# Performance work log

Measured on AMD Instinct MI355X. Metric: run time of the kernel, lower is better.

Reference implementation:

```python
import jax, jax.numpy as jnp
import numpy as np
import math

B, N, D, H = 4, 2048, 1024, 16
HD = D // H  # head dim = 64


def setup_inputs() -> dict:
    key = jax.random.key(0)
    ks = jax.random.split(key, 5)
    x = jax.random.normal(ks[0], (B, N, D), dtype=jnp.float32)
    # per-head kqv Linear: weight (3*HD, D), bias (3*HD), stacked over heads
    Wkqv = jax.random.normal(ks[1], (H, 3 * HD, D), dtype=jnp.float32) / math.sqrt(D)
    bkqv = jax.random.normal(ks[2], (H, 3 * HD), dtype=jnp.float32) * 0.02
    # output projection Linear(D, D)
    Wproj = jax.random.normal(ks[3], (D, D), dtype=jnp.float32) / math.sqrt(D)
    bproj = jax.random.normal(ks[4], (D,), dtype=jnp.float32) * 0.02
    return {"x": x, "Wkqv": Wkqv, "bkqv": bkqv, "Wproj": Wproj, "bproj": bproj}


def reference(x, Wkqv, bkqv, Wproj, bproj):
    # per-head linear: y = x @ W.T + b  -> [B, H, N, 3*HD]
    kqv = jnp.einsum('bnd,hed->bhne', x, Wkqv) + bkqv[None, :, None, :]
    k, q, v = jnp.split(kqv, 3, axis=-1)  # each [B, H, N, HD]
    # scores = q @ k^T / sqrt(HD)   (attention_scores(k, q) -> q @ k.T)
    scores = jnp.einsum('bhqd,bhkd->bhqk', q, k) / math.sqrt(HD)
    causal = jnp.tril(jnp.ones((N, N), dtype=bool))
    scores = jnp.where(causal[None, None], scores, -jnp.inf)
    att = jax.nn.softmax(scores, axis=-1)
    out = jnp.einsum('bhqk,bhkd->bhqd', att, v)  # [B, H, N, HD]
    # concat heads: [B, N, H*HD]
    sa = out.transpose(0, 2, 1, 3).reshape(B, N, D)
    # dropout is identity in eval mode; final projection
    return sa @ Wproj.T + bproj
```

## Files before the change

kernel.cpp:

```cpp
#include <hip/hip_runtime.h>
#include <hip/hip_bf16.h>


#define NSEQ 2048
#define NHEAD 16
#define DMODEL 1024
#define SCALE2 0.18033688011112042f

typedef __attribute__((ext_vector_type(8))) short v8s;
typedef __attribute__((ext_vector_type(4))) float v4f;

__device__ __forceinline__ float bf2f(unsigned short u) {
    union { unsigned int i; float f; } v;
    v.i = ((unsigned int)u) << 16;
    return v.f;
}
__device__ __forceinline__ unsigned short f2bf(float f) {
    unsigned int x = __float_as_uint(f);
    return (unsigned short)((x + 0x7fffu + ((x >> 16) & 1u)) >> 16);
}
__device__ __forceinline__ unsigned short f2bf_rh(float f) {
    return (unsigned short)((__float_as_uint(f) + 0x8000u) >> 16);
}
__device__ __forceinline__ float fast_exp2(float x) {
#if __has_builtin(__builtin_amdgcn_exp2f)
    return __builtin_amdgcn_exp2f(x);
#else
    return __expf(x * 0.69314718056f);
#endif
}
__device__ __forceinline__ void gld_lds16(const unsigned short* g, unsigned short* l) {
    __builtin_amdgcn_global_load_lds(
        (const __attribute__((address_space(1))) void*)g,
        (__attribute__((address_space(3))) void*)l, 16, 0, 0);
}

__global__ __launch_bounds__(256) void cvt_bf16(
    const float* __restrict__ x, const float* __restrict__ wk, const float* __restrict__ wp,
    unsigned short* __restrict__ xb, unsigned short* __restrict__ wkb,
    unsigned short* __restrict__ wpb)
{
    const int i = blockIdx.x * 256 + threadIdx.x;
    const float* s; unsigned short* d; int o;
    if (i < 2097152)      { s = x;  d = xb;  o = i; }
    else if (i < 2883584) {
        s = wk; d = wkb;
        const int oi  = i - 2097152;
        const int row = oi >> 8, cq = oi & 255;
        const int h   = row / 192;
        const int rem = row - h * 192;
        const int cls = rem >> 6, e = rem & 63;
        float4 f = ((const float4*)s)[oi];
        ushort4 u;
        u.x = f2bf(f.x); u.y = f2bf(f.y); u.z = f2bf(f.z); u.w = f2bf(f.w);
        ((ushort4*)d)[(((cls << 10) + (h << 6) + e) << 8) + cq] = u;
        return;
    }
    else                  { s = wp; d = wpb; o = i - 2883584; }
    float4 f = ((const float4*)s)[o];
    ushort4 u;
    u.x = f2bf(f.x); u.y = f2bf(f.y); u.z = f2bf(f.z); u.w = f2bf(f.w);
    ((ushort4*)d)[o] = u;
}

template <int EPI>
__global__ __launch_bounds__(256, 3) void gemm_lds(
    const unsigned short* __restrict__ A, const unsigned short* __restrict__ B,
    const float* __restrict__ bias,
    float* __restrict__ Cf,
    unsigned short* __restrict__ Kb, unsigned short* __restrict__ Qb,
    unsigned short* __restrict__ VTb,
    int M, int Nc, int K)
{
    __shared__ __align__(16) unsigned short Al[512 * 8];
    __shared__ __align__(16) unsigned short Bl[512 * 8];

    const int t = threadIdx.x, wave = t >> 6, lane = t & 63;
    const int wm = wave >> 1, wn = wave & 1;
    const int m0 = blockIdx.y * 128, n0 = blockIdx.x * 128;
    const int quad = lane >> 4, c = lane & 15;

    const int g0 = wave * 2, g1 = wave * 2 + 1;
    const int r15 = lane & 15, kg = (lane >> 4) & 3;
    const unsigned short* sA0 = A + (size_t)(m0 + g0 * 16 + r15) * K + kg * 8;
    const unsigned short* sA1 = A + (size_t)(m0 + g1 * 16 + r15) * K + kg * 8;
    const unsigned short* sB0 = B + (size_t)(n0 + g0 * 16 + r15) * K + kg * 8;
    const unsigned short* sB1 = B + (size_t)(n0 + g1 * 16 + r15) * K + kg * 8;
    unsigned short* dA0 = &Al[g0 * 512];
    unsigned short* dA1 = &Al[g1 * 512];
    unsigned short* dB0 = &Bl[g0 * 512];
    unsigned short* dB1 = &Bl[g1 * 512];

    v4f acc[4][4];
#pragma unroll
    for (int i = 0; i < 4; ++i)
#pragma unroll
        for (int j = 0; j < 4; ++j) acc[i][j] = (v4f){0.f, 0.f, 0.f, 0.f};

    const int fbase = (quad * 16 + c) * 8;

    for (int k0 = 0; k0 < K; k0 += 32) {
        __syncthreads();
        gld_lds16(sA0 + k0, dA0);
        gld_lds16(sA1 + k0, dA1);
        gld_lds16(sB0 + k0, dB0);
        gld_lds16(sB1 + k0, dB1);
        __syncthreads();

        v8s af[4], bf[4];
#pragma unroll
        for (int ms = 0; ms < 4; ++ms)
            af[ms] = *(const v8s*)&Al[(wm * 4 + ms) * 512 + fbase];
#pragma unroll
        for (int ns = 0; ns < 4; ++ns)
            bf[ns] = *(const v8s*)&Bl[(wn * 4 + ns) * 512 + fbase];
#pragma unroll
        for (int ms = 0; ms < 4; ++ms)
#pragma unroll
            for (int ns = 0; ns < 4; ++ns)
                acc[ms][ns] = __builtin_amdgcn_mfma_f32_16x16x32_bf16(
                    af[ms], bf[ns], acc[ms][ns], 0, 0, 0);
    }

#pragma unroll
    for (int ms = 0; ms < 4; ++ms) {
        const int row0 = m0 + wm * 64 + ms * 16 + quad * 4;
#pragma unroll
        for (int ns = 0; ns < 4; ++ns) {
            const int colbase = n0 + wn * 64 + ns * 16;
            float bn, scl = 1.f;
            if (EPI == 2) {
                bn = bias[colbase + c];
            } else {
                const int cls = colbase >> 10;
                const int wi  = colbase & 1023;
                const int h   = wi >> 6, e0 = wi & 63;
                bn = bias[h * 192 + cls * 64 + e0 + c];
                if (cls == 1) scl = SCALE2;
            }
            float v0 = (acc[ms][ns][0] + bn) * scl;
            float v1 = (acc[ms][ns][1] + bn) * scl;
            float v2 = (acc[ms][ns][2] + bn) * scl;
            float v3 = (acc[ms][ns][3] + bn) * scl;
            if (EPI == 2) {
                float* pc = Cf + (size_t)row0 * Nc + colbase + c;
                pc[0] = v0; pc[(size_t)Nc] = v1;
                pc[(size_t)2 * Nc] = v2; pc[(size_t)3 * Nc] = v3;
            } else {
                const int cls = colbase >> 10;
                const int wi  = colbase & 1023;
                const int h   = wi >> 6, e = (wi & 63) + c;
                const int bb  = row0 >> 11, tok0 = row0 & 2047;
                const int bhh = bb * 16 + h;
                if (cls == 2) {
                    ushort4 pk;
                    pk.x = f2bf(v0); pk.y = f2bf(v1); pk.z = f2bf(v2); pk.w = f2bf(v3);
                    *(ushort4*)(VTb + ((size_t)bhh * 64 + e) * 2048 + tok0) = pk;
                } else {
                    unsigned short* dst = (cls == 0) ? Kb : Qb;
                    const size_t base = ((size_t)bhh * 2048 + tok0) * 64 + e;
                    dst[base]       = f2bf(v0);
                    dst[base + 64]  = f2bf(v1);
                    dst[base + 128] = f2bf(v2);
                    dst[base + 192] = f2bf(v3);
                }
            }
        }
    }
}

template <bool A_BF16, int EPI>
__global__ __launch_bounds__(256) void gemm_mfma(
    const void* __restrict__ Av, const float* __restrict__ B,
    const float* __restrict__ bias,
    float* __restrict__ Cf,
    unsigned short* __restrict__ Kb, unsigned short* __restrict__ Qb,
    unsigned short* __restrict__ VTb,
    int M, int Nc, int K)
{
    __shared__ __align__(16) unsigned short Al[512 * 8];
    __shared__ __align__(16) unsigned short Bl[512 * 8];

    const int t = threadIdx.x;
    const int wave = t >> 6, lane = t & 63;
    const int wm = wave >> 1, wn = wave & 1;
    const int m0 = blockIdx.y * 128, n0 = blockIdx.x * 128;
    const int quad = lane >> 4, c = lane & 15;

    const int srow = t >> 1, skh = t & 1;
    const int sslot = (srow >> 4) * 64 + (skh * 2) * 16 + (srow & 15);

    v4f acc[4][4];
#pragma unroll
    for (int i = 0; i < 4; ++i)
#pragma unroll
        for (int j = 0; j < 4; ++j) acc[i][j] = (v4f){0.f, 0.f, 0.f, 0.f};

    const unsigned short* pa_u = (const unsigned short*)Av + (size_t)(m0 + srow) * K + skh * 16;
    const float*          pa_f = (const float*)Av          + (size_t)(m0 + srow) * K + skh * 16;
    const float*          pb   = B                          + (size_t)(n0 + srow) * K + skh * 16;

    const int fbase = (quad * 16 + c) * 8;

    for (int k0 = 0; k0 < K; k0 += 32) {
        unsigned short a16[16], b16[16];
        if (A_BF16) {
            uint4 r0 = *(const uint4*)(pa_u + k0);
            uint4 r1 = *(const uint4*)(pa_u + k0 + 8);
            *(uint4*)&a16[0] = r0; *(uint4*)&a16[8] = r1;
        } else {
            float4 f0 = *(const float4*)(pa_f + k0);
            float4 f1 = *(const float4*)(pa_f + k0 + 4);
            float4 f2 = *(const float4*)(pa_f + k0 + 8);
            float4 f3 = *(const float4*)(pa_f + k0 + 12);
            a16[0] = f2bf_rh(f0.x); a16[1] = f2bf_rh(f0.y); a16[2] = f2bf_rh(f0.z); a16[3] = f2bf_rh(f0.w);
            a16[4] = f2bf_rh(f1.x); a16[5] = f2bf_rh(f1.y); a16[6] = f2bf_rh(f1.z); a16[7] = f2bf_rh(f1.w);
            a16[8] = f2bf_rh(f2.x); a16[9] = f2bf_rh(f2.y); a16[10] = f2bf_rh(f2.z); a16[11] = f2bf_rh(f2.w);
            a16[12] = f2bf_rh(f3.x); a16[13] = f2bf_rh(f3.y); a16[14] = f2bf_rh(f3.z); a16[15] = f2bf_rh(f3.w);
        }
        {
            float4 g0 = *(const float4*)(pb + k0);
            float4 g1 = *(const float4*)(pb + k0 + 4);
            float4 g2 = *(const float4*)(pb + k0 + 8);
            float4 g3 = *(const float4*)(pb + k0 + 12);
            b16[0] = f2bf_rh(g0.x); b16[1] = f2bf_rh(g0.y); b16[2] = f2bf_rh(g0.z); b16[3] = f2bf_rh(g0.w);
            b16[4] = f2bf_rh(g1.x); b16[5] = f2bf_rh(g1.y); b16[6] = f2bf_rh(g1.z); b16[7] = f2bf_rh(g1.w);
            b16[8] = f2bf_rh(g2.x); b16[9] = f2bf_rh(g2.y); b16[10] = f2bf_rh(g2.z); b16[11] = f2bf_rh(g2.w);
            b16[12] = f2bf_rh(g3.x); b16[13] = f2bf_rh(g3.y); b16[14] = f2bf_rh(g3.z); b16[15] = f2bf_rh(g3.w);
        }
        __syncthreads();
        *(uint4*)&Al[sslot * 8]        = *(uint4*)&a16[0];
        *(uint4*)&Al[(sslot + 16) * 8] = *(uint4*)&a16[8];
        *(uint4*)&Bl[sslot * 8]        = *(uint4*)&b16[0];
        *(uint4*)&Bl[(sslot + 16) * 8] = *(uint4*)&b16[8];
        __syncthreads();

        v8s af[4], bf[4];
#pragma unroll
        for (int ms = 0; ms < 4; ++ms)
            af[ms] = *(const v8s*)&Al[(wm * 4 + ms) * 512 + fbase];
#pragma unroll
        for (int ns = 0; ns < 4; ++ns)
            bf[ns] = *(const v8s*)&Bl[(wn * 4 + ns) * 512 + fbase];
#pragma unroll
        for (int ms = 0; ms < 4; ++ms)
#pragma unroll
            for (int ns = 0; ns < 4; ++ns)
                acc[ms][ns] = __builtin_amdgcn_mfma_f32_16x16x32_bf16(
                    af[ms], bf[ns], acc[ms][ns], 0, 0, 0);
    }

#pragma unroll
    for (int ms = 0; ms < 4; ++ms) {
        const int row0 = m0 + wm * 64 + ms * 16 + quad * 4;
#pragma unroll
        for (int ns = 0; ns < 4; ++ns) {
            const int colbase = n0 + wn * 64 + ns * 16;
            float bn = (EPI == 2) ? bias[colbase + c] : bias[colbase + c];
            float v0 = acc[ms][ns][0] + bn;
            float v1 = acc[ms][ns][1] + bn;
            float v2 = acc[ms][ns][2] + bn;
            float v3 = acc[ms][ns][3] + bn;
            if (EPI == 2) {
                float* pc = Cf + (size_t)row0 * Nc + colbase + c;
                pc[0] = v0; pc[(size_t)Nc] = v1;
                pc[(size_t)2 * Nc] = v2; pc[(size_t)3 * Nc] = v3;
            } else {
                const int hh = colbase / 192;
                const int eb = colbase - hh * 192;
                const int bb = row0 >> 11, tok0 = row0 & 2047;
                const int bhh = bb * 16 + hh;
                if (eb >= 128) {
                    ushort4 pk;
                    pk.x = f2bf(v0); pk.y = f2bf(v1); pk.z = f2bf(v2); pk.w = f2bf(v3);
                    *(ushort4*)(VTb + ((size_t)bhh * 64 + (eb - 128) + c) * 2048 + tok0) = pk;
                } else {
                    const bool isq = (eb >= 64);
                    const float s = isq ? SCALE2 : 1.f;
                    unsigned short* dst = isq ? Qb : Kb;
                    const int e = (isq ? eb - 64 : eb) + c;
                    const size_t base = ((size_t)bhh * 2048 + tok0) * 64 + e;
                    dst[base]       = f2bf(v0 * s);
                    dst[base + 64]  = f2bf(v1 * s);
                    dst[base + 128] = f2bf(v2 * s);
                    dst[base + 192] = f2bf(v3 * s);
                }
            }
        }
    }
}

#define ATTS 72

__global__ __launch_bounds__(256, 2) void attn_mfma(
    const unsigned short* __restrict__ Kbuf,
    const unsigned short* __restrict__ Qbuf,
    const unsigned short* __restrict__ VT,
    unsigned short* __restrict__ sa)
{
    __shared__ __align__(16) unsigned short Ps[4][64 * ATTS];

    const int t = threadIdx.x, w = t >> 6, lane = t & 63;
    const int quad = lane >> 4, c = lane & 15;
    const int bh = blockIdx.x & 63, bq = blockIdx.x >> 6;
    const int b = bh >> 4, hh = bh & 15;
    const int qt = (w == 0) ? bq : (w == 1) ? (15 - bq) : (w == 2) ? (16 + bq) : (31 - bq);
    const int qw = qt * 64;
    const size_t gbase = (size_t)bh * (2048 * 64);

    const int rs  = c & 3;
    const int rc0 = (quad ^ rs) * 8, rc1 = 32 + rc0;
    unsigned short* PsW = &Ps[w][0];

    v8s qf[4][2];
#pragma unroll
    for (int qs = 0; qs < 4; ++qs) {
        const unsigned short* qp = Qbuf + gbase + (size_t)(qw + qs * 16 + c) * 64 + quad * 8;
        qf[qs][0] = *(const v8s*)qp;
        qf[qs][1] = *(const v8s*)(qp + 32);
    }
    v4f oacc[4][4], lacc[4];
#pragma unroll
    for (int qs = 0; qs < 4; ++qs) {
        lacc[qs] = (v4f){0.f, 0.f, 0.f, 0.f};
#pragma unroll
        for (int dn = 0; dn < 4; ++dn) oacc[qs][dn] = (v4f){0.f, 0.f, 0.f, 0.f};
    }
    const short oneb = (short)0x3F80;
    const v8s ones = {oneb, oneb, oneb, oneb, oneb, oneb, oneb, oneb};

    const int nkt = qt + 1;
    for (int kt = 0; kt < nkt; ++kt) {
        const int kbase = kt * 64;
        const bool diag = (kt == nkt - 1);
#pragma unroll
        for (int kn = 0; kn < 4; ++kn) {
            const unsigned short* kp =
                Kbuf + gbase + (size_t)(kbase + kn * 16 + c) * 64 + quad * 8;
            v8s kf0 = *(const v8s*)kp;
            v8s kf1 = *(const v8s*)(kp + 32);
#pragma unroll
            for (int qs = 0; qs < 4; ++qs) {
                v4f s = (v4f){0.f, 0.f, 0.f, 0.f};
                s = __builtin_amdgcn_mfma_f32_16x16x32_bf16(qf[qs][0], kf0, s, 0, 0, 0);
                s = __builtin_amdgcn_mfma_f32_16x16x32_bf16(qf[qs][1], kf1, s, 0, 0, 0);
                if (diag) {
#pragma unroll
                    for (int r = 0; r < 4; ++r)
                        if (kn * 16 + c > qs * 16 + quad * 4 + r) s[r] = -1e30f;
                }
#pragma unroll
                for (int r = 0; r < 4; ++r) {
                    const float p = fast_exp2(s[r]);
                    PsW[(qs * 16 + quad * 4 + r) * ATTS +
                        (((2 * kn + (c >> 3)) ^ r) * 8) + (c & 7)] = f2bf_rh(p);
                }
            }
        }
        v8s pa[4][2];
#pragma unroll
        for (int qs = 0; qs < 4; ++qs) {
            pa[qs][0] = *(const v8s*)&PsW[(qs * 16 + c) * ATTS + rc0];
            pa[qs][1] = *(const v8s*)&PsW[(qs * 16 + c) * ATTS + rc1];
        }
#pragma unroll
        for (int dn = 0; dn < 4; ++dn) {
            const unsigned short* vp =
                VT + gbase + (size_t)(dn * 16 + c) * 2048 + kbase + quad * 8;
            v8s vf0 = *(const v8s*)vp;
            v8s vf1 = *(const v8s*)(vp + 32);
#pragma unroll
            for (int qs = 0; qs < 4; ++qs) {
                oacc[qs][dn] = __builtin_amdgcn_mfma_f32_16x16x32_bf16(pa[qs][0], vf0, oacc[qs][dn], 0, 0, 0);
                oacc[qs][dn] = __builtin_amdgcn_mfma_f32_16x16x32_bf16(pa[qs][1], vf1, oacc[qs][dn], 0, 0, 0);
            }
        }
#pragma unroll
        for (int qs = 0; qs < 4; ++qs) {
            lacc[qs] = __builtin_amdgcn_mfma_f32_16x16x32_bf16(pa[qs][0], ones, lacc[qs], 0, 0, 0);
            lacc[qs] = __builtin_amdgcn_mfma_f32_16x16x32_bf16(pa[qs][1], ones, lacc[qs], 0, 0, 0);
        }
    }

#pragma unroll
    for (int qs = 0; qs < 4; ++qs) {
        float inv[4];
#pragma unroll
        for (int r = 0; r < 4; ++r) inv[r] = 1.f / lacc[qs][r];
        const size_t obase =
            ((size_t)(b * 2048 + qw + qs * 16 + quad * 4)) * DMODEL + hh * 64;
#pragma unroll
        for (int dn = 0; dn < 4; ++dn)
#pragma unroll
            for (int r = 0; r < 4; ++r)
                sa[obase + (size_t)r * DMODEL + dn * 16 + c] = f2bf(oacc[qs][dn][r] * inv[r]);
    }
}

extern "C" void kernel_launch(void* const* d_in, const int* in_sizes, int n_in,
                              void* d_out, int out_size, void* d_ws, size_t ws_size,
                              hipStream_t stream) {
    const float* x     = (const float*)d_in[0];
    const float* Wkqv  = (const float*)d_in[1];
    const float* bkqv  = (const float*)d_in[2];
    const float* Wproj = (const float*)d_in[3];
    const float* bproj = (const float*)d_in[4];
    float* out = (float*)d_out;

    unsigned short* Kb = (unsigned short*)d_ws;
    unsigned short* Qb = Kb + (size_t)8388608;
    unsigned short* VT = Qb + (size_t)8388608;
    unsigned short* sa = VT + (size_t)8388608;

    const bool fast = ws_size >= 75497472ull;
    if (fast) {
        unsigned short* xb  = sa;
        unsigned short* wkb = (unsigned short*)d_ws + (size_t)33554432;
        unsigned short* wpb = wkb + (size_t)3145728;
        cvt_bf16<<<12288, 256, 0, stream>>>(x, Wkqv, Wproj, xb, wkb, wpb);
        gemm_lds<1><<<dim3(24, 64), 256, 0, stream>>>(
            xb, wkb, bkqv, nullptr, Kb, Qb, VT, 8192, 3072, 1024);
        attn_mfma<<<512, 256, 0, stream>>>(Kb, Qb, VT, sa);
        gemm_lds<2><<<dim3(8, 64), 256, 0, stream>>>(
            sa, wpb, bproj, out, nullptr, nullptr, nullptr, 8192, 1024, 1024);
    } else {
        gemm_mfma<false, 1><<<dim3(24, 64), 256, 0, stream>>>(
            x, Wkqv, bkqv, nullptr, Kb, Qb, VT, 8192, 3072, 1024);
        attn_mfma<<<512, 256, 0, stream>>>(Kb, Qb, VT, sa);
        gemm_mfma<true, 2><<<dim3(8, 64), 256, 0, stream>>>(
            sa, Wproj, bproj, out, nullptr, nullptr, nullptr, 8192, 1024, 1024);
    }
}
```

Before: 333.8 us.

## Triple-buffer GEMM LDS loads and remap blocks for XCD locality

The GEMM main loop moves from a single LDS buffer with two barriers per k-step to a three-stage ring. Global-to-LDS loads for tile k+2 are issued before computing tile k, and explicit vmcnt waits plus one barrier per step keep them ordered. Block indices are also remapped so that consecutive blocks on the same XCD share nearby M rows, which should improve L2 reuse. LDS use per block triples, which may reduce occupancy. The swizzle assumes gridDim.y is a multiple of 64 rows grouped per XCD, so it depends on the grid shape.

```diff
diff --git a/kernel.cpp b/kernel.cpp
--- a/kernel.cpp
+++ b/kernel.cpp
@@ -72,12 +72,17 @@
     unsigned short* __restrict__ VTb,
     int M, int Nc, int K)
 {
-    __shared__ __align__(16) unsigned short Al[512 * 8];
-    __shared__ __align__(16) unsigned short Bl[512 * 8];
+    __shared__ __align__(16) unsigned short Al[3][4096];
+    __shared__ __align__(16) unsigned short Bl[3][4096];
 
     const int t = threadIdx.x, wave = t >> 6, lane = t & 63;
     const int wm = wave >> 1, wn = wave & 1;
-    const int m0 = blockIdx.y * 128, n0 = blockIdx.x * 128;
+
+    const int lin = blockIdx.y * gridDim.x + blockIdx.x;
+    const int xcd = lin & 7, pos = lin >> 3;
+    const int by  = (xcd << 3) + (pos & 7);
+    const int bx  = pos >> 3;
+    const int m0 = by * 128, n0 = bx * 128;
     const int quad = lane >> 4, c = lane & 15;
 
     const int g0 = wave * 2, g1 = wave * 2 + 1;
@@ -86,10 +91,6 @@
     const unsigned short* sA1 = A + (size_t)(m0 + g1 * 16 + r15) * K + kg * 8;
     const unsigned short* sB0 = B + (size_t)(n0 + g0 * 16 + r15) * K + kg * 8;
     const unsigned short* sB1 = B + (size_t)(n0 + g1 * 16 + r15) * K + kg * 8;
-    unsigned short* dA0 = &Al[g0 * 512];
-    unsigned short* dA1 = &Al[g1 * 512];
-    unsigned short* dB0 = &Bl[g0 * 512];
-    unsigned short* dB1 = &Bl[g1 * 512];
 
     v4f acc[4][4];
 #pragma unroll
@@ -98,28 +99,48 @@
         for (int j = 0; j < 4; ++j) acc[i][j] = (v4f){0.f, 0.f, 0.f, 0.f};
 
     const int fbase = (quad * 16 + c) * 8;
-
-    for (int k0 = 0; k0 < K; k0 += 32) {
-        __syncthreads();
-        gld_lds16(sA0 + k0, dA0);
-        gld_lds16(sA1 + k0, dA1);
-        gld_lds16(sB0 + k0, dB0);
-        gld_lds16(sB1 + k0, dB1);
-        __syncthreads();
-
-        v8s af[4], bf[4];
+    const int nt = K >> 5;
+
+    auto stage = [&](int b, int tt) {
+        const int o = tt << 5;
+        unsigned short* la = &Al[b][0];
+        unsigned short* lb = &Bl[b][0];
+        gld_lds16(sA0 + o, la + g0 * 512);
+        gld_lds16(sA1 + o, la + g1 * 512);
+        gld_lds16(sB0 + o, lb + g0 * 512);
+        gld_lds16(sB1 + o, lb + g1 * 512);
+    };
+
+    stage(0, 0);
+    stage(1, 1);
+    asm volatile("s_waitcnt vmcnt(4)" ::: "memory");
+    __builtin_amdgcn_s_barrier();
+
+    int cur = 0;
+    for (int tt = 0; tt < nt; ++tt) {
+        const int nxt = (cur == 2) ? 0 : cur + 1;
+        const int b2  = (nxt == 2) ? 0 : nxt + 1;
+        const bool pf = (tt + 2 < nt);
+        if (pf) stage(b2, tt + 2);
+
+        v8s af[4], bfr[4];
 #pragma unroll
         for (int ms = 0; ms < 4; ++ms)
-            af[ms] = *(const v8s*)&Al[(wm * 4 + ms) * 512 + fbase];
+            af[ms] = *(const v8s*)&Al[cur][(wm * 4 + ms) * 512 + fbase];
 #pragma unroll
         for (int ns = 0; ns < 4; ++ns)
-            bf[ns] = *(const v8s*)&Bl[(wn * 4 + ns) * 512 + fbase];
+            bfr[ns] = *(const v8s*)&Bl[cur][(wn * 4 + ns) * 512 + fbase];
 #pragma unroll
         for (int ms = 0; ms < 4; ++ms)
 #pragma unroll
             for (int ns = 0; ns < 4; ++ns)
                 acc[ms][ns] = __builtin_amdgcn_mfma_f32_16x16x32_bf16(
-                    af[ms], bf[ns], acc[ms][ns], 0, 0, 0);
+                    af[ms], bfr[ns], acc[ms][ns], 0, 0, 0);
+
+        if (pf) { asm volatile("s_waitcnt vmcnt(4)" ::: "memory"); }
+        else    { asm volatile("s_waitcnt vmcnt(0)" ::: "memory"); }
+        __builtin_amdgcn_s_barrier();
+        cur = nxt;
     }
 
 #pragma unroll
```

Measured after the change: 318.2 us. 1.05x faster.
